# Kernel optimization log

Hardware: AMD Instinct MI355X
Metric: run time of the kernel (lower is better)

Reference implementation:

```python
import jax, jax.numpy as jnp
import numpy as np

B, S, HID = 4, 2048, 768
NH, DH = 12, 64          # num heads, per-head attention_size
AHS = NH * DH            # all_head_size
EPS = 1e-5


def setup_inputs() -> dict:
    key = jax.random.key(0)
    ks = jax.random.split(key, 12)
    sd = 0.02
    return {
        "hidden_states": jax.random.normal(ks[0], (B, S, HID), jnp.float32),
        "attention_mask": jnp.ones((B, S), jnp.float32),
        "Wq": jax.random.normal(ks[1], (HID, AHS), jnp.float32) * sd,
        "bq": jnp.zeros((AHS,), jnp.float32),
        "Wk": jax.random.normal(ks[2], (HID, AHS), jnp.float32) * sd,
        "bk": jnp.zeros((AHS,), jnp.float32),
        "Wv": jax.random.normal(ks[3], (HID, AHS), jnp.float32) * sd,
        "bv": jnp.zeros((AHS,), jnp.float32),
        "Wo": jax.random.normal(ks[4], (AHS, HID), jnp.float32) * sd,
        "bo": jnp.zeros((HID,), jnp.float32),
        "ln_g": jnp.ones((HID,), jnp.float32),
        "ln_b": jnp.zeros((HID,), jnp.float32),
    }


def reference(hidden_states, attention_mask, Wq, bq, Wk, bk, Wv, bv, Wo, bo, ln_g, ln_b):
    x = hidden_states
    # QKV projections -> (B, S, NH, DH)
    q = (x @ Wq + bq).reshape(B, S, NH, DH)
    k = (x @ Wk + bk).reshape(B, S, NH, DH)
    v = (x @ Wv + bv).reshape(B, S, NH, DH)
    # scaled dot-product scores (B, NH, S, S)
    scores = jnp.einsum("bqhd,bkhd->bhqk", q, k) / jnp.sqrt(jnp.float32(DH))
    # mask: (B, S) -> additive bias on key axis
    scores = scores + ((1.0 - attention_mask) * -10000.0)[:, None, None, :]
    probs = jax.nn.softmax(scores, axis=-1)  # dropout = identity (eval)
    ctx = jnp.einsum("bhqk,bkhd->bqhd", probs, v).reshape(B, S, AHS)
    out = ctx @ Wo + bo  # dropout = identity (eval)
    # residual + LayerNorm
    y = out + x
    mu = jnp.mean(y, axis=-1, keepdims=True)
    var = jnp.mean(jnp.square(y - mu), axis=-1, keepdims=True)
    return (y - mu) * jax.lax.rsqrt(var + EPS) * ln_g + ln_b
```

## Files before the change

kernel.cpp:

```cpp
#include <hip/hip_runtime.h>
#include <cstdint>

typedef __bf16 bf16x8 __attribute__((ext_vector_type(8)));
typedef float f32x4 __attribute__((ext_vector_type(4)));
typedef float f32x16 __attribute__((ext_vector_type(16)));

#define NHEADS 12
#define BATCH 4
#define SEQ 2048
#define HID 768
#define DHEAD 64
#define TOTHEADS 48
#define MROWS 8192
#define LOG2E 1.4426950408889634f

__device__ __forceinline__ ushort f2bf(float f) {
  union { float f; uint32_t u; } v; v.f = f;
  uint32_t u = v.u;
  uint32_t r = (u + 0x7fffu + ((u >> 16) & 1u)) >> 16;
  return (ushort)r;
}

__device__ __forceinline__ float bf2f(ushort u) {
  union { uint32_t u; float f; } v; v.u = (uint32_t)u << 16; return v.f;
}

__device__ __forceinline__ void gload_lds16(const void* g, void* l) {
  __builtin_amdgcn_global_load_lds((const __attribute__((address_space(1))) void*)g,
                                   (__attribute__((address_space(3))) void*)l, 16, 0, 0);
}

__device__ __forceinline__ float xor32_max(float x) {
  float t = x;
  asm("v_permlane32_swap_b32 %0, %1" : "+v"(t), "+v"(x));
  return fmaxf(t, x);
}
__device__ __forceinline__ float xor32_add(float x) {
  float t = x;
  asm("v_permlane32_swap_b32 %0, %1" : "+v"(t), "+v"(x));
  return t + x;
}

__global__ void cvt_x_kernel(const float* __restrict__ x, ushort* __restrict__ xb,
                             const float* __restrict__ mask, float* __restrict__ biasArr) {
  int bid = blockIdx.x;
  if (bid < 6144) {
    int i = bid * 256 + threadIdx.x;
    const float4 v = *reinterpret_cast<const float4*>(&x[(size_t)i * 4]);
    ushort4 o;
    o.x = f2bf(v.x); o.y = f2bf(v.y); o.z = f2bf(v.z); o.w = f2bf(v.w);
    *reinterpret_cast<ushort4*>(&xb[(size_t)i * 4]) = o;
  } else {
    int i = (bid - 6144) * 256 + threadIdx.x;
    const float4 mv = *reinterpret_cast<const float4*>(&mask[(size_t)i * 4]);
    float4 bv;
    bv.x = (1.0f - mv.x) * -10000.0f * LOG2E;
    bv.y = (1.0f - mv.y) * -10000.0f * LOG2E;
    bv.z = (1.0f - mv.z) * -10000.0f * LOG2E;
    bv.w = (1.0f - mv.w) * -10000.0f * LOG2E;
    *reinterpret_cast<float4*>(&biasArr[(size_t)i * 4]) = bv;
  }
}

__global__ void transpose_all_kernel(const float* __restrict__ W0, const float* __restrict__ W1,
                                     const float* __restrict__ W2, const float* __restrict__ W3,
                                     ushort* __restrict__ wqkvT, ushort* __restrict__ woT) {
  __shared__ float tile[32][33];
  int z = blockIdx.z;
  const float* W = (z == 0) ? W0 : (z == 1) ? W1 : (z == 2) ? W2 : W3;
  ushort* Wt = (z == 3) ? woT : wqkvT + (size_t)z * HID * HID;
  int bx = blockIdx.x * 32;
  int by = blockIdx.y * 32;
  int tx = threadIdx.x, ty = threadIdx.y;
#pragma unroll
  for (int i = 0; i < 32; i += 8)
    tile[ty + i][tx] = W[(size_t)(by + ty + i) * HID + bx + tx];
  __syncthreads();
#pragma unroll
  for (int i = 0; i < 32; i += 8)
    Wt[(size_t)(bx + ty + i) * HID + by + tx] = f2bf(tile[tx][ty + i]);
}

__device__ __forceinline__ void gemm_mainloop(const ushort* __restrict__ A,
                                              const ushort* __restrict__ Bt,
                                              int row0, int col0,
                                              ushort* As, ushort* Bs,
                                              f32x4 (&acc)[4][4], int wv, int lane) {
  const int RW = (wv >> 1) * 64, CW = (wv & 1) * 64;
  const int rr = wv * 16 + (lane >> 2);
  const int cc = (lane & 3) * 8;
  const ushort* A0 = A + (size_t)(row0 + rr) * 768 + cc;
  const ushort* A1 = A + (size_t)(row0 + 64 + rr) * 768 + cc;
  const ushort* B0 = Bt + (size_t)(col0 + rr) * 768 + cc;
  const ushort* B1 = Bt + (size_t)(col0 + 64 + rr) * 768 + cc;
  gload_lds16(A0, As + (wv * 16) * 32);
  gload_lds16(A1, As + (64 + wv * 16) * 32);
  gload_lds16(B0, Bs + (wv * 16) * 32);
  gload_lds16(B1, Bs + (64 + wv * 16) * 32);
  __syncthreads();
  for (int k0 = 0; k0 < 768; k0 += 32) {
    const int buf = (k0 >> 5) & 1;
    if (k0 + 32 < 768) {
      ushort* AsN = As + (buf ^ 1) * (128 * 32);
      ushort* BsN = Bs + (buf ^ 1) * (128 * 32);
      gload_lds16(A0 + k0 + 32, AsN + (wv * 16) * 32);
      gload_lds16(A1 + k0 + 32, AsN + (64 + wv * 16) * 32);
      gload_lds16(B0 + k0 + 32, BsN + (wv * 16) * 32);
      gload_lds16(B1 + k0 + 32, BsN + (64 + wv * 16) * 32);
    }
    const ushort* AsB = As + buf * (128 * 32);
    const ushort* BsB = Bs + buf * (128 * 32);
    bf16x8 a[4], b[4];
#pragma unroll
    for (int m = 0; m < 4; ++m)
      a[m] = *reinterpret_cast<const bf16x8*>(&AsB[(RW + m * 16 + (lane & 15)) * 32 + (lane >> 4) * 8]);
#pragma unroll
    for (int n = 0; n < 4; ++n)
      b[n] = *reinterpret_cast<const bf16x8*>(&BsB[(CW + n * 16 + (lane & 15)) * 32 + (lane >> 4) * 8]);
    __builtin_amdgcn_s_setprio(1);
#pragma unroll
    for (int m = 0; m < 4; ++m)
#pragma unroll
      for (int n = 0; n < 4; ++n)
        acc[m][n] = __builtin_amdgcn_mfma_f32_16x16x32_bf16(a[m], b[n], acc[m][n], 0, 0, 0);
    __builtin_amdgcn_s_setprio(0);
    __syncthreads();
  }
}

__global__ __launch_bounds__(256) void gemm_qkv_kernel(const ushort* __restrict__ A,
                                                       const ushort* __restrict__ Bt,
                                                       const float* __restrict__ bq,
                                                       const float* __restrict__ bk,
                                                       const float* __restrict__ bv,
                                                       ushort* __restrict__ Qo,
                                                       ushort* __restrict__ Ko,
                                                       ushort* __restrict__ Vto) {
  __shared__ ushort As[2 * 128 * 32];
  __shared__ ushort Bs[2 * 128 * 32];
  int tid = threadIdx.x, wv = tid >> 6, lane = tid & 63;
  int row0 = blockIdx.x * 128, col0 = blockIdx.y * 128;
  f32x4 acc[4][4] = {};
  gemm_mainloop(A, Bt, row0, col0, As, Bs, acc, wv, lane);

  const int RW = (wv >> 1) * 64, CW = (wv & 1) * 64;
#pragma unroll
  for (int m = 0; m < 4; ++m)
#pragma unroll
    for (int n = 0; n < 4; ++n) {
      int col = col0 + CW + n * 16 + (lane & 15);
      int t = col / 768, rem = col % 768;
      int hh = rem / 64, d = rem % 64;
      const float* bias = (t == 0) ? bq : ((t == 1) ? bk : bv);
      float bvv = bias[rem];
      int row_base = row0 + RW + m * 16 + (lane >> 4) * 4;
      int bb = row_base >> 11;
      int s0 = row_base & 2047;
      int head = bb * NHEADS + hh;
      if (t == 2) {
        ushort4 vv;
        vv.x = f2bf(acc[m][n][0] + bvv);
        vv.y = f2bf(acc[m][n][1] + bvv);
        vv.z = f2bf(acc[m][n][2] + bvv);
        vv.w = f2bf(acc[m][n][3] + bvv);
        *reinterpret_cast<ushort4*>(&Vto[((size_t)head * DHEAD + d) * SEQ + s0]) = vv;
      } else {
        ushort* dst = (t == 0) ? Qo : Ko;
        float scl = (t == 0) ? (0.125f * LOG2E) : 1.0f;
#pragma unroll
        for (int j = 0; j < 4; ++j)
          dst[((size_t)head * SEQ + s0 + j) * DHEAD + d] = f2bf((acc[m][n][j] + bvv) * scl);
      }
    }
}

__global__ __launch_bounds__(256) void gemm_out_kernel(const ushort* __restrict__ A,
                                                       const ushort* __restrict__ Bt,
                                                       const float* __restrict__ bo,
                                                       ushort* __restrict__ tmpb) {
  __shared__ ushort As[2 * 128 * 32];
  __shared__ ushort Bs[2 * 128 * 32];
  int tid = threadIdx.x, wv = tid >> 6, lane = tid & 63;
  int row0 = blockIdx.x * 128, col0 = blockIdx.y * 128;
  f32x4 acc[4][4] = {};
  gemm_mainloop(A, Bt, row0, col0, As, Bs, acc, wv, lane);

  const int RW = (wv >> 1) * 64, CW = (wv & 1) * 64;
#pragma unroll
  for (int m = 0; m < 4; ++m)
#pragma unroll
    for (int n = 0; n < 4; ++n) {
      int col = col0 + CW + n * 16 + (lane & 15);
      float bvv = bo[col];
      int row_base = row0 + RW + m * 16 + (lane >> 4) * 4;
#pragma unroll
      for (int j = 0; j < 4; ++j)
        tmpb[(size_t)(row_base + j) * HID + col] = f2bf(acc[m][n][j] + bvv);
    }
}

__device__ __forceinline__ void stage_kv(const ushort*& kp0, const ushort*& kp1,
                                         const ushort* vp0, const ushort* vp1, int k0,
                                         ushort* Kd, ushort* Vd, int wb) {
  gload_lds16(kp0, Kd + wb * 64);
  gload_lds16(kp1, Kd + (wb + 8) * 64);
  gload_lds16(vp0 + k0, Vd + wb * 64);
  gload_lds16(vp1 + k0, Vd + (wb + 8) * 64);
  kp0 += 64 * DHEAD; kp1 += 64 * DHEAD;
}

__device__ __forceinline__ void attn_tile(const ushort* __restrict__ KsB,
                                          const ushort* __restrict__ VsB,
                                          const float* __restrict__ biasL, int k0,
                                          const bf16x8 (&bq)[4], bool bz,
                                          f32x16 (&accO)[2], float& mrun, float& lrun,
                                          int lo, int hi) {
  f32x16 ps[2];
  if (bz) {
#pragma unroll
    for (int kb = 0; kb < 2; ++kb)
#pragma unroll
      for (int r = 0; r < 16; ++r) ps[kb][r] = 0.f;
  } else {
#pragma unroll
    for (int kb = 0; kb < 2; ++kb)
#pragma unroll
      for (int g = 0; g < 4; ++g) {
        const float4 bb = *reinterpret_cast<const float4*>(&biasL[k0 + kb * 32 + g * 8 + hi * 4]);
        ps[kb][g * 4 + 0] = bb.x; ps[kb][g * 4 + 1] = bb.y;
        ps[kb][g * 4 + 2] = bb.z; ps[kb][g * 4 + 3] = bb.w;
      }
  }
  __builtin_amdgcn_s_setprio(1);
#pragma unroll
  for (int kb = 0; kb < 2; ++kb) {
    int key = kb * 32 + lo;
#pragma unroll
    for (int kd = 0; kd < 4; ++kd) {
      bf16x8 ak = *reinterpret_cast<const bf16x8*>(
          &KsB[key * 64 + ((kd * 16 + hi * 8) ^ ((key & 7) << 3))]);
      ps[kb] = __builtin_amdgcn_mfma_f32_32x32x16_bf16(ak, bq[kd], ps[kb], 0, 0, 0);
    }
  }
  __builtin_amdgcn_s_setprio(0);

  bf16x8 av[2][2][2];
#pragma unroll
  for (int nb = 0; nb < 2; ++nb) {
    int d = nb * 32 + lo;
#pragma unroll
    for (int kb = 0; kb < 2; ++kb)
#pragma unroll
      for (int kk = 0; kk < 2; ++kk)
        av[nb][kb][kk] = *reinterpret_cast<const bf16x8*>(
            &VsB[d * 64 + ((kb * 32 + kk * 16 + hi * 8) ^ ((d & 7) << 3))]);
  }

  float mx[8];
#pragma unroll
  for (int i = 0; i < 8; ++i)
    mx[i] = fmaxf(fmaxf(ps[0][i], ps[0][i + 8]), fmaxf(ps[1][i], ps[1][i + 8]));
  float m01 = fmaxf(fmaxf(mx[0], mx[1]), mx[2]);
  float m23 = fmaxf(fmaxf(mx[3], mx[4]), mx[5]);
  float rm = fmaxf(fmaxf(m01, m23), fmaxf(mx[6], mx[7]));
  rm = xor32_max(rm);

  if (!__all(rm <= mrun + 8.f)) {
    float mnew = fmaxf(mrun, rm);
    float scl = exp2f(mrun - mnew);
    mrun = mnew;
    lrun *= scl;
#pragma unroll
    for (int nb = 0; nb < 2; ++nb)
#pragma unroll
      for (int r = 0; r < 16; ++r) accO[nb][r] *= scl;
  }

#pragma unroll
  for (int kb = 0; kb < 2; ++kb)
#pragma unroll
    for (int r = 0; r < 16; ++r)
      ps[kb][r] = exp2f(ps[kb][r] - mrun);

  float sm[8];
#pragma unroll
  for (int i = 0; i < 8; ++i)
    sm[i] = (ps[0][i] + ps[0][i + 8]) + (ps[1][i] + ps[1][i + 8]);
  float rs = ((sm[0] + sm[1]) + (sm[2] + sm[3])) + ((sm[4] + sm[5]) + (sm[6] + sm[7]));
  rs = xor32_add(rs);
  lrun += rs;

  __builtin_amdgcn_s_setprio(1);
#pragma unroll
  for (int kb = 0; kb < 2; ++kb) {
    uint w[8];
#pragma unroll
    for (int i = 0; i < 8; ++i) {
      float a0 = ps[kb][2 * i], a1 = ps[kb][2 * i + 1];
      asm("v_cvt_pk_bf16_f32 %0, %1, %2" : "=v"(w[i]) : "v"(a0), "v"(a1));
    }
    asm("v_permlane32_swap_b32 %0, %1" : "+v"(w[0]), "+v"(w[2]));
    asm("v_permlane32_swap_b32 %0, %1" : "+v"(w[1]), "+v"(w[3]));
    asm("v_permlane32_swap_b32 %0, %1" : "+v"(w[4]), "+v"(w[6]));
    asm("v_permlane32_swap_b32 %0, %1" : "+v"(w[5]), "+v"(w[7]));
    uint4 u0 = make_uint4(w[0], w[1], w[2], w[3]);
    uint4 u1 = make_uint4(w[4], w[5], w[6], w[7]);
    bf16x8 pa0 = __builtin_bit_cast(bf16x8, u0);
    bf16x8 pa1 = __builtin_bit_cast(bf16x8, u1);
#pragma unroll
    for (int nb = 0; nb < 2; ++nb) {
      accO[nb] = __builtin_amdgcn_mfma_f32_32x32x16_bf16(av[nb][kb][0], pa0, accO[nb], 0, 0, 0);
      accO[nb] = __builtin_amdgcn_mfma_f32_32x32x16_bf16(av[nb][kb][1], pa1, accO[nb], 0, 0, 0);
    }
  }
  __builtin_amdgcn_s_setprio(0);
}

__global__ __launch_bounds__(256, 3) void attn_kernel(const ushort* __restrict__ Q,
                                                      const ushort* __restrict__ Kg,
                                                      const ushort* __restrict__ Vt,
                                                      const float* __restrict__ biasArr,
                                                      ushort* __restrict__ ctx) {
  __shared__ ushort Ks[2][64 * 64];
  __shared__ ushort Vs[2][64 * 64];
  __shared__ float biasL[SEQ];

  int tid = threadIdx.x, wv = tid >> 6, lane = tid & 63;
  int lo = lane & 31, hi = lane >> 5;

  int bid = blockIdx.x;
  int x = bid & 7, j = bid >> 3;
  int hh = x * 6 + (j >> 4);
  int qt = j & 15;
  int b = hh / NHEADS, h = hh % NHEADS;
  int q0w = qt * 128 + wv * 32;

  const ushort* Qh = Q + (size_t)hh * SEQ * DHEAD;
  const ushort* Kh = Kg + (size_t)hh * SEQ * DHEAD;
  const ushort* Vh = Vt + (size_t)hh * DHEAD * SEQ;
  const float* brow = biasArr + (size_t)b * SEQ;

  int r8 = lane >> 3, sc = ((lane & 7) ^ r8) * 8;
  int wb = wv * 16;
  const ushort* kp0 = Kh + (size_t)(wb + r8) * DHEAD + sc;
  const ushort* kp1 = kp0 + (size_t)8 * DHEAD;
  const ushort* vp0 = Vh + (size_t)(wb + r8) * SEQ + sc;
  const ushort* vp1 = vp0 + (size_t)8 * SEQ;

#pragma unroll
  for (int c = 0; c < 2; ++c) {
    int chunk = wv * 2 + c;
    gload_lds16(brow + chunk * 256 + lane * 4, biasL + chunk * 256);
  }

  bf16x8 bq[4];
#pragma unroll
  for (int kd = 0; kd < 4; ++kd)
    bq[kd] = *reinterpret_cast<const bf16x8*>(&Qh[(size_t)(q0w + lo) * DHEAD + kd * 16 + hi * 8]);

  f32x16 accO[2] = {};
  float mrun = -1e30f, lrun = 0.f;

  stage_kv(kp0, kp1, vp0, vp1, 0, Ks[0], Vs[0], wb);
  __syncthreads();

  float bsum = 0.f;
#pragma unroll
  for (int i = 0; i < 2; ++i) {
    const float4 bb = *reinterpret_cast<const float4*>(&biasL[(tid * 2 + i) * 4]);
    bsum += (fabsf(bb.x) + fabsf(bb.y)) + (fabsf(bb.z) + fabsf(bb.w));
  }
  bool bz = __syncthreads_and(bsum == 0.f) != 0;

  for (int k0 = 0; k0 < SEQ; k0 += 128) {
    stage_kv(kp0, kp1, vp0, vp1, k0 + 64, Ks[1], Vs[1], wb);
    attn_tile(Ks[0], Vs[0], biasL, k0, bq, bz, accO, mrun, lrun, lo, hi);
    __syncthreads();
    if (k0 + 128 < SEQ)
      stage_kv(kp0, kp1, vp0, vp1, k0 + 128, Ks[0], Vs[0], wb);
    attn_tile(Ks[1], Vs[1], biasL, k0 + 64, bq, bz, accO, mrun, lrun, lo, hi);
    __syncthreads();
  }

  float inv = 1.0f / lrun;
  size_t rowbase = ((size_t)(b * SEQ) + q0w + lo) * HID + h * DHEAD;
#pragma unroll
  for (int nb = 0; nb < 2; ++nb)
#pragma unroll
    for (int g = 0; g < 4; ++g) {
      ushort4 o;
      o.x = f2bf(accO[nb][g * 4 + 0] * inv);
      o.y = f2bf(accO[nb][g * 4 + 1] * inv);
      o.z = f2bf(accO[nb][g * 4 + 2] * inv);
      o.w = f2bf(accO[nb][g * 4 + 3] * inv);
      int d = nb * 32 + g * 8 + hi * 4;
      *reinterpret_cast<ushort4*>(&ctx[rowbase + d]) = o;
    }
}

__global__ __launch_bounds__(256) void ln_kernel(const ushort* __restrict__ tmpb,
                                                 const ushort* __restrict__ xb,
                                                 const float* __restrict__ g,
                                                 const float* __restrict__ bta,
                                                 float* __restrict__ out) {
  int wv = threadIdx.x >> 6, lane = threadIdx.x & 63;
  int row = blockIdx.x * 4 + wv;
  const ushort* tr = tmpb + (size_t)row * HID;
  const ushort* xr = xb + (size_t)row * HID;
  float v[12];
  float s = 0.f, ss = 0.f;
#pragma unroll
  for (int i = 0; i < 3; ++i) {
    int c = i * 256 + lane * 4;
    ushort4 tv = *reinterpret_cast<const ushort4*>(&tr[c]);
    ushort4 xv = *reinterpret_cast<const ushort4*>(&xr[c]);
    float a0 = bf2f(tv.x) + bf2f(xv.x);
    float a1 = bf2f(tv.y) + bf2f(xv.y);
    float a2 = bf2f(tv.z) + bf2f(xv.z);
    float a3 = bf2f(tv.w) + bf2f(xv.w);
    v[i * 4 + 0] = a0; v[i * 4 + 1] = a1; v[i * 4 + 2] = a2; v[i * 4 + 3] = a3;
    s += (a0 + a1) + (a2 + a3);
    ss += (a0 * a0 + a1 * a1) + (a2 * a2 + a3 * a3);
  }
#pragma unroll
  for (int msk = 1; msk < 64; msk <<= 1) {
    s += __shfl_xor(s, msk);
    ss += __shfl_xor(ss, msk);
  }
  float mu = s * (1.f / HID);
  float var = ss * (1.f / HID) - mu * mu;
  float inv = rsqrtf(var + 1e-5f);
  float* orow = out + (size_t)row * HID;
#pragma unroll
  for (int i = 0; i < 3; ++i) {
    int c = i * 256 + lane * 4;
    const float4 gv = *reinterpret_cast<const float4*>(&g[c]);
    const float4 bv = *reinterpret_cast<const float4*>(&bta[c]);
    float4 ov;
    ov.x = (v[i * 4 + 0] - mu) * inv * gv.x + bv.x;
    ov.y = (v[i * 4 + 1] - mu) * inv * gv.y + bv.y;
    ov.z = (v[i * 4 + 2] - mu) * inv * gv.z + bv.z;
    ov.w = (v[i * 4 + 3] - mu) * inv * gv.w + bv.w;
    *reinterpret_cast<float4*>(&orow[c]) = ov;
  }
}

extern "C" void kernel_launch(void* const* d_in, const int* in_sizes, int n_in,
                              void* d_out, int out_size, void* d_ws, size_t ws_size,
                              hipStream_t stream) {
  const float* x    = (const float*)d_in[0];
  const float* mask = (const float*)d_in[1];
  const float* Wq   = (const float*)d_in[2];
  const float* bq   = (const float*)d_in[3];
  const float* Wk   = (const float*)d_in[4];
  const float* bk   = (const float*)d_in[5];
  const float* Wv   = (const float*)d_in[6];
  const float* bv   = (const float*)d_in[7];
  const float* Wo   = (const float*)d_in[8];
  const float* bo   = (const float*)d_in[9];
  const float* lng  = (const float*)d_in[10];
  const float* lnb  = (const float*)d_in[11];
  float* out = (float*)d_out;

  char* w = (char*)d_ws;
  size_t o = 0;
  ushort* xb    = (ushort*)(w + o); o += (size_t)MROWS * HID * 2;
  ushort* wqkvT = (ushort*)(w + o); o += (size_t)3 * HID * HID * 2;
  ushort* woT   = (ushort*)(w + o); o += (size_t)HID * HID * 2;
  size_t qb_off = o;
  ushort* Qb    = (ushort*)(w + o); o += (size_t)TOTHEADS * SEQ * DHEAD * 2;
  ushort* Kb    = (ushort*)(w + o); o += (size_t)TOTHEADS * SEQ * DHEAD * 2;
  ushort* Vtb   = (ushort*)(w + o); o += (size_t)TOTHEADS * SEQ * DHEAD * 2;
  ushort* ctx   = (ushort*)(w + o); o += (size_t)MROWS * HID * 2;
  float* biasArr = (float*)(w + o); o += (size_t)BATCH * SEQ * 4;
  ushort* tmpb  = (ushort*)(w + qb_off);

  cvt_x_kernel<<<6152, 256, 0, stream>>>(x, xb, mask, biasArr);
  dim3 tb(32, 8), tg3(HID / 32, HID / 32, 4);
  transpose_all_kernel<<<tg3, tb, 0, stream>>>(Wq, Wk, Wv, Wo, wqkvT, woT);

  gemm_qkv_kernel<<<dim3(MROWS / 128, 2304 / 128), 256, 0, stream>>>(
      xb, wqkvT, bq, bk, bv, Qb, Kb, Vtb);

  attn_kernel<<<TOTHEADS * 16, 256, 0, stream>>>(Qb, Kb, Vtb, biasArr, ctx);

  gemm_out_kernel<<<dim3(MROWS / 128, HID / 128), 256, 0, stream>>>(ctx, woT, bo, tmpb);

  ln_kernel<<<MROWS / 4, 256, 0, stream>>>(tmpb, xb, lng, lnb, out);
}
```

Before: 178.1 us.

## Compute softmax row sums via MFMA with ones and fold max into accumulator init

Replaces the per-tile VALU row-sum reduction and lane swap with two extra MFMAs per key block that multiply the bf16 probabilities by a ones matrix, accumulating the softmax denominator in a matrix accumulator. It also folds the running max subtraction into the QK MFMA initial accumulator (cinit = -mrun) or the bias preload, so the exp2 no longer needs a subtract. This trades VALU work on the softmax path for extra MFMA issue and an extra 16-register accumulator. The denominator is now summed from bf16-rounded probabilities, which matches what is actually multiplied into V.

```diff
diff --git a/kernel.cpp b/kernel.cpp
--- a/kernel.cpp
+++ b/kernel.cpp
@@ -34,11 +34,6 @@
   float t = x;
   asm("v_permlane32_swap_b32 %0, %1" : "+v"(t), "+v"(x));
   return fmaxf(t, x);
-}
-__device__ __forceinline__ float xor32_add(float x) {
-  float t = x;
-  asm("v_permlane32_swap_b32 %0, %1" : "+v"(t), "+v"(x));
-  return t + x;
 }
 
 __global__ void cvt_x_kernel(const float* __restrict__ x, ushort* __restrict__ xb,
@@ -212,34 +207,39 @@
 __device__ __forceinline__ void attn_tile(const ushort* __restrict__ KsB,
                                           const ushort* __restrict__ VsB,
                                           const float* __restrict__ biasL, int k0,
-                                          const bf16x8 (&bq)[4], bool bz,
-                                          f32x16 (&accO)[2], float& mrun, float& lrun,
+                                          const bf16x8 (&bq)[4], const bf16x8 ones, bool bz,
+                                          f32x16 (&accO)[2], f32x16& accL,
+                                          f32x16& cinit, float& mrun,
                                           int lo, int hi) {
   f32x16 ps[2];
+  __builtin_amdgcn_s_setprio(1);
   if (bz) {
 #pragma unroll
-    for (int kb = 0; kb < 2; ++kb)
-#pragma unroll
-      for (int r = 0; r < 16; ++r) ps[kb][r] = 0.f;
+    for (int kb = 0; kb < 2; ++kb) {
+      int key = kb * 32 + lo;
+#pragma unroll
+      for (int kd = 0; kd < 4; ++kd) {
+        bf16x8 ak = *reinterpret_cast<const bf16x8*>(
+            &KsB[key * 64 + ((kd * 16 + hi * 8) ^ ((key & 7) << 3))]);
+        ps[kb] = __builtin_amdgcn_mfma_f32_32x32x16_bf16(ak, bq[kd], (kd == 0) ? cinit : ps[kb], 0, 0, 0);
+      }
+    }
   } else {
 #pragma unroll
-    for (int kb = 0; kb < 2; ++kb)
+    for (int kb = 0; kb < 2; ++kb) {
 #pragma unroll
       for (int g = 0; g < 4; ++g) {
         const float4 bb = *reinterpret_cast<const float4*>(&biasL[k0 + kb * 32 + g * 8 + hi * 4]);
-        ps[kb][g * 4 + 0] = bb.x; ps[kb][g * 4 + 1] = bb.y;
-        ps[kb][g * 4 + 2] = bb.z; ps[kb][g * 4 + 3] = bb.w;
+        ps[kb][g * 4 + 0] = bb.x - mrun; ps[kb][g * 4 + 1] = bb.y - mrun;
+        ps[kb][g * 4 + 2] = bb.z - mrun; ps[kb][g * 4 + 3] = bb.w - mrun;
       }
-  }
-  __builtin_amdgcn_s_setprio(1);
-#pragma unroll
-  for (int kb = 0; kb < 2; ++kb) {
-    int key = kb * 32 + lo;
-#pragma unroll
-    for (int kd = 0; kd < 4; ++kd) {
-      bf16x8 ak = *reinterpret_cast<const bf16x8*>(
-          &KsB[key * 64 + ((kd * 16 + hi * 8) ^ ((key & 7) << 3))]);
-      ps[kb] = __builtin_amdgcn_mfma_f32_32x32x16_bf16(ak, bq[kd], ps[kb], 0, 0, 0);
+      int key = kb * 32 + lo;
+#pragma unroll
+      for (int kd = 0; kd < 4; ++kd) {
+        bf16x8 ak = *reinterpret_cast<const bf16x8*>(
+            &KsB[key * 64 + ((kd * 16 + hi * 8) ^ ((key & 7) << 3))]);
+        ps[kb] = __builtin_amdgcn_mfma_f32_32x32x16_bf16(ak, bq[kd], ps[kb], 0, 0, 0);
+      }
     }
   }
   __builtin_amdgcn_s_setprio(0);
@@ -265,30 +265,25 @@
   float rm = fmaxf(fmaxf(m01, m23), fmaxf(mx[6], mx[7]));
   rm = xor32_max(rm);
 
-  if (!__all(rm <= mrun + 8.f)) {
-    float mnew = fmaxf(mrun, rm);
-    float scl = exp2f(mrun - mnew);
-    mrun = mnew;
-    lrun *= scl;
-#pragma unroll
-    for (int nb = 0; nb < 2; ++nb)
-#pragma unroll
-      for (int r = 0; r < 16; ++r) accO[nb][r] *= scl;
+  if (!__all(rm <= 8.f)) {
+    float d = fmaxf(rm, 0.f);
+    float scl = exp2f(-d);
+    mrun += d;
+#pragma unroll
+    for (int r = 0; r < 16; ++r) cinit[r] = -mrun;
+#pragma unroll
+    for (int kb = 0; kb < 2; ++kb)
+#pragma unroll
+      for (int r = 0; r < 16; ++r) ps[kb][r] -= d;
+#pragma unroll
+    for (int r = 0; r < 16; ++r) { accO[0][r] *= scl; accO[1][r] *= scl; accL[r] *= scl; }
   }
 
 #pragma unroll
   for (int kb = 0; kb < 2; ++kb)
 #pragma unroll
     for (int r = 0; r < 16; ++r)
-      ps[kb][r] = exp2f(ps[kb][r] - mrun);
-
-  float sm[8];
-#pragma unroll
-  for (int i = 0; i < 8; ++i)
-    sm[i] = (ps[0][i] + ps[0][i + 8]) + (ps[1][i] + ps[1][i + 8]);
-  float rs = ((sm[0] + sm[1]) + (sm[2] + sm[3])) + ((sm[4] + sm[5]) + (sm[6] + sm[7]));
-  rs = xor32_add(rs);
-  lrun += rs;
+      ps[kb][r] = exp2f(ps[kb][r]);
 
   __builtin_amdgcn_s_setprio(1);
 #pragma unroll
@@ -312,6 +307,8 @@
       accO[nb] = __builtin_amdgcn_mfma_f32_32x32x16_bf16(av[nb][kb][0], pa0, accO[nb], 0, 0, 0);
       accO[nb] = __builtin_amdgcn_mfma_f32_32x32x16_bf16(av[nb][kb][1], pa1, accO[nb], 0, 0, 0);
     }
+    accL = __builtin_amdgcn_mfma_f32_32x32x16_bf16(ones, pa0, accL, 0, 0, 0);
+    accL = __builtin_amdgcn_mfma_f32_32x32x16_bf16(ones, pa1, accL, 0, 0, 0);
   }
   __builtin_amdgcn_s_setprio(0);
 }
@@ -358,8 +355,13 @@
   for (int kd = 0; kd < 4; ++kd)
     bq[kd] = *reinterpret_cast<const bf16x8*>(&Qh[(size_t)(q0w + lo) * DHEAD + kd * 16 + hi * 8]);
 
+  uint oo = 0x3f803f80u;
+  bf16x8 ones = __builtin_bit_cast(bf16x8, make_uint4(oo, oo, oo, oo));
+
   f32x16 accO[2] = {};
-  float mrun = -1e30f, lrun = 0.f;
+  f32x16 accL = {};
+  f32x16 cinit = {};
+  float mrun = 0.f;
 
   stage_kv(kp0, kp1, vp0, vp1, 0, Ks[0], Vs[0], wb);
   __syncthreads();
@@ -374,15 +376,15 @@
 
   for (int k0 = 0; k0 < SEQ; k0 += 128) {
     stage_kv(kp0, kp1, vp0, vp1, k0 + 64, Ks[1], Vs[1], wb);
-    attn_tile(Ks[0], Vs[0], biasL, k0, bq, bz, accO, mrun, lrun, lo, hi);
+    attn_tile(Ks[0], Vs[0], biasL, k0, bq, ones, bz, accO, accL, cinit, mrun, lo, hi);
     __syncthreads();
     if (k0 + 128 < SEQ)
       stage_kv(kp0, kp1, vp0, vp1, k0 + 128, Ks[0], Vs[0], wb);
-    attn_tile(Ks[1], Vs[1], biasL, k0 + 64, bq, bz, accO, mrun, lrun, lo, hi);
+    attn_tile(Ks[1], Vs[1], biasL, k0 + 64, bq, ones, bz, accO, accL, cinit, mrun, lo, hi);
     __syncthreads();
   }
 
-  float inv = 1.0f / lrun;
+  float inv = 1.0f / accL[0];
   size_t rowbase = ((size_t)(b * SEQ) + q0w + lo) * HID + h * DHEAD;
 #pragma unroll
   for (int nb = 0; nb < 2; ++nb)
```

Result: slower. 199.0 us (+11.7%).
